# Optimization experiments

Hardware: AMD Instinct MI355X
Metric: run time of the kernel (lower is better)

The kernel has to match this reference:

```python
import jax, jax.numpy as jnp
import numpy as np

ALPHA = 0.2  # LeakyReLU negative slope
NEG = -9e15

def _gat_head(Wh, a1, a2, adj_mask):
    # Wh: [N,O], a1/a2: [O], adj_mask: [N,N] bool
    e = jax.nn.leaky_relu(jnp.einsum('no,o->n', Wh, a1)[:, None]
                          + jnp.einsum('no,o->n', Wh, a2)[None, :], ALPHA)
    att = jax.nn.softmax(jnp.where(adj_mask, e, NEG), axis=-1)
    return att @ Wh  # [N,O]

def setup_inputs() -> dict:
    key = jax.random.key(0)
    ks = jax.random.split(key, 6)
    N, F_IN, O, H, C = 4096, 512, 64, 8, 16
    x = jax.random.normal(ks[0], (N, F_IN), jnp.float32)
    adj = jax.random.randint(ks[1], (N, N), 0, 2, jnp.int32)
    W = jax.random.normal(ks[2], (H, F_IN, O), jnp.float32) * 0.05
    a = jax.random.normal(ks[3], (H, 2 * O), jnp.float32) * 0.05
    W_out = jax.random.normal(ks[4], (H * O, C), jnp.float32) * 0.05
    a_out = jax.random.normal(ks[5], (2 * C,), jnp.float32) * 0.05
    return {'x': x, 'adj': adj, 'W': W, 'a': a, 'W_out': W_out, 'a_out': a_out}

def reference(x, adj, W, a, W_out, a_out):
    N = x.shape[0]
    H, _, O = W.shape
    C = W_out.shape[1]
    mask = adj > 0  # [N,N]
    # multi-head attention layer (vmapped over heads)
    Wh = jnp.einsum('nf,hfo->hno', x, W)  # [H,N,O]
    a1, a2 = a[:, :O], a[:, O:]
    h_heads = jax.vmap(_gat_head, in_axes=(0, 0, 0, None))(Wh, a1, a2, mask)  # [H,N,O]
    h = jax.nn.elu(h_heads)  # concat=True -> elu per head
    h = jnp.transpose(h, (1, 0, 2)).reshape(N, H * O)  # concat heads
    # output attention layer (concat=False)
    Wh_o = h @ W_out  # [N,C]
    out = _gat_head(Wh_o, a_out[:C], a_out[C:], mask)  # [N,C]
    out = jax.nn.elu(out)
    return jax.nn.log_softmax(out, axis=1)
```

## Files before the change

### kernel.cpp

```cpp
#include <hip/hip_runtime.h>


typedef __attribute__((ext_vector_type(8))) short short8;
typedef __attribute__((ext_vector_type(4))) float f32x4;
typedef unsigned long long u64;
typedef unsigned short u16;
typedef unsigned int u32;

__device__ __forceinline__ u16 f2bf_rne(float f){
  u32 u = __float_as_uint(f);
  return (u16)((u + 0x7fffu + ((u >> 16) & 1u)) >> 16);
}
__device__ __forceinline__ void async16(void* lds, const void* g){
  __builtin_amdgcn_global_load_lds((const __attribute__((address_space(1))) u32*)g,
                                   (__attribute__((address_space(3))) u32*)lds, 16, 0, 0);
}

__global__ __launch_bounds__(256) void k_prep(const float* __restrict__ x,
                                              const float* __restrict__ W,
                                              u16* __restrict__ xA,
                                              u16* __restrict__ wB){
  if (blockIdx.x < 1024){
    int t = blockIdx.x * 256 + threadIdx.x;
    int n = t & 4095, fg = t >> 12;
    const float* src = x + (size_t)n * 512 + fg * 8;
    float4 v0 = ((const float4*)src)[0];
    float4 v1 = ((const float4*)src)[1];
    u32 pk[4];
    pk[0] = f2bf_rne(v0.x) | ((u32)f2bf_rne(v0.y) << 16);
    pk[1] = f2bf_rne(v0.z) | ((u32)f2bf_rne(v0.w) << 16);
    pk[2] = f2bf_rne(v1.x) | ((u32)f2bf_rne(v1.y) << 16);
    pk[3] = f2bf_rne(v1.z) | ((u32)f2bf_rne(v1.w) << 16);
    *(uint4*)(xA + ((size_t)fg * 4096 + n) * 8) = *(uint4*)pk;
  } else {
    int t = (blockIdx.x - 1024) * 256 + threadIdx.x;
    int o = t & 63, fg = (t >> 6) & 63, h = t >> 12;
    const float* src = W + ((size_t)h * 512 + fg * 8) * 64 + o;
    u32 pk[4];
    #pragma unroll
    for (int p = 0; p < 4; ++p){
      u16 lo = f2bf_rne(src[(2 * p) * 64]);
      u16 hi = f2bf_rne(src[(2 * p + 1) * 64]);
      pk[p] = lo | ((u32)hi << 16);
    }
    *(uint4*)(wB + (size_t)h * 32768 + ((size_t)fg * 64 + o) * 8) = *(uint4*)pk;
  }
}

__global__ __launch_bounds__(256) void k_gemm1(const u16* __restrict__ xA,
                                               const u16* __restrict__ wB,
                                               const float* __restrict__ av,
                                               const int* __restrict__ adj,
                                               u16* __restrict__ whB,
                                               u64* __restrict__ bits_t,
                                               float* __restrict__ r1,
                                               float* __restrict__ e21, float* __restrict__ e202){
  __shared__ u16 tr[4096];
  int h    = blockIdx.y;
  int nblk = blockIdx.x;
  int lane = threadIdx.x & 63;
  int wv   = threadIdx.x >> 6;
  int row16 = lane & 15, grp = lane >> 4;
  int n0 = nblk * 64;
  int n0w = n0 + wv * 16;
  const u16* wBh = wB + (size_t)h * 32768;
  f32x4 acc[4] = {};
  #pragma unroll 4
  for (int ks = 0; ks < 16; ++ks){
    int fgb = ks * 4 + grp;
    short8 af = *(const short8*)(xA + ((size_t)fgb * 4096 + n0w + row16) * 8);
    #pragma unroll
    for (int nt = 0; nt < 4; ++nt){
      short8 bf = *(const short8*)(wBh + ((size_t)fgb * 64 + nt * 16 + row16) * 8);
      acc[nt] = __builtin_amdgcn_mfma_f32_16x16x32_bf16(af, bf, acc[nt], 0, 0, 0);
    }
  }
  float a1v[4], a2v[4];
  #pragma unroll
  for (int nt = 0; nt < 4; ++nt){
    a1v[nt] = av[h * 128 + nt * 16 + row16];
    a2v[nt] = av[h * 128 + 64 + nt * 16 + row16];
  }
  #pragma unroll
  for (int r = 0; r < 4; ++r){
    float p1 = acc[0][r]*a1v[0] + acc[1][r]*a1v[1] + acc[2][r]*a1v[2] + acc[3][r]*a1v[3];
    float p2 = acc[0][r]*a2v[0] + acc[1][r]*a2v[1] + acc[2][r]*a2v[2] + acc[3][r]*a2v[3];
    #pragma unroll
    for (int d = 1; d < 16; d <<= 1){ p1 += __shfl_xor(p1, d, 64); p2 += __shfl_xor(p2, d, 64); }
    if (row16 == 0){
      int idx = h * 4096 + n0w + grp * 4 + r;
      r1[idx]   = __expf(-0.8f * p1);
      e21[idx]  = __expf(p2);
      e202[idx] = __expf(0.2f * p2);
    }
  }
  #pragma unroll
  for (int nt = 0; nt < 4; ++nt)
    #pragma unroll
    for (int r = 0; r < 4; ++r){
      int jl = wv * 16 + grp * 4 + r;
      int o  = nt * 16 + row16;
      tr[((jl >> 3) * 64 + o) * 8 + (jl & 7)] = f2bf_rne(acc[nt][r]);
    }
  __syncthreads();
  u16* dst = whB + (size_t)h * 262144 + (size_t)n0 * 64;
  #pragma unroll
  for (int q = 0; q < 2; ++q)
    *(uint4*)(dst + (threadIdx.x * 2 + q) * 8) = *(const uint4*)(tr + (threadIdx.x * 2 + q) * 8);

  {
    int B = blockIdx.y * 64 + blockIdx.x;
    int uid0 = B * 512 + wv * 128;
    for (int k = 0; k < 128; k += 8){
      int v[8];
      #pragma unroll
      for (int q = 0; q < 8; ++q){
        int uid = uid0 + k + q;
        v[q] = adj[(size_t)(uid >> 6) * 4096 + ((uid & 63) << 6) + lane];
      }
      u64 m[8];
      #pragma unroll
      for (int q = 0; q < 8; ++q) m[q] = __ballot(v[q] != 0);
      if (lane == 0){
        #pragma unroll
        for (int q = 0; q < 8; ++q){
          int uid = uid0 + k + q;
          bits_t[(size_t)(uid & 63) * 4096 + (uid >> 6)] = m[q];
        }
      }
    }
  }
}

__global__ __launch_bounds__(256) void k_att1(const u16* __restrict__ whB,
                                              const u64* __restrict__ bits_t,
                                              const float* __restrict__ r1,
                                              const float* __restrict__ e21, const float* __restrict__ e202,
                                              u16* __restrict__ pnum, float* __restrict__ pden){
  __shared__ u16  smB[2][4096];
  __shared__ u32  smLut[4];
  int h     = blockIdx.y;
  int iblk  = blockIdx.x;
  int split = blockIdx.z;
  int lane = threadIdx.x & 63;
  int wv   = threadIdx.x >> 6;
  int row16 = lane & 15, grp = lane >> 4;
  if (threadIdx.x < 4)
    smLut[threadIdx.x] = ((threadIdx.x & 1) ? 0xFFFFu : 0u) | ((threadIdx.x & 2) ? 0xFFFF0000u : 0u);
  int i = iblk * 64 + wv * 16 + row16;
  int hoff = h * 4096;
  float r = r1[hoff + i];
  const u16* whBh = whB + (size_t)h * 262144;
  int jbeg = split * 1024;

  short8 bden;
  #pragma unroll
  for (int t = 0; t < 8; ++t) bden[t] = (row16 == 0) ? (short)0x3F80 : (short)0;

  auto stage = [&](int bb, int j0){
    const char* g = (const char*)whBh + (size_t)j0 * 128 + wv * 2048 + lane * 16;
    char* l = (char*)(&smB[bb][0]) + wv * 2048;
    async16(l, g);
    async16(l + 1024, g + 1024);
  };

  f32x4 acc[4] = {};
  f32x4 accden = {};
  stage(0, jbeg);
  for (int c = 0; c < 16; ++c){
    int bb = c & 1;
    int j0 = jbeg + c * 64;
    u64 mrow = bits_t[(size_t)(split * 16 + c) * 4096 + i];
    __syncthreads();
    if (c < 15) stage(bb ^ 1, j0 + 64);
    #pragma unroll
    for (int ks = 0; ks < 2; ++ks){
      const float* t1 = e21  + hoff + j0 + ks * 32 + grp * 8;
      const float* t2 = e202 + hoff + j0 + ks * 32 + grp * 8;
      float4 eA = *(const float4*)t1;
      float4 eB = *(const float4*)(t1 + 4);
      float4 gA = *(const float4*)t2;
      float4 gB = *(const float4*)(t2 + 4);
      float e1v[8] = {eA.x, eA.y, eA.z, eA.w, eB.x, eB.y, eB.z, eB.w};
      float e2v[8] = {gA.x, gA.y, gA.z, gA.w, gB.x, gB.y, gB.z, gB.w};
      const u16* bbase = &smB[bb][(ks * 4 + grp) * 512];
      short8 bf0 = *(const short8*)(bbase + (0 * 16 + row16) * 8);
      short8 bf1 = *(const short8*)(bbase + (1 * 16 + row16) * 8);
      short8 bf2 = *(const short8*)(bbase + (2 * 16 + row16) * 8);
      short8 bf3 = *(const short8*)(bbase + (3 * 16 + row16) * 8);
      u32 mb = ((u32)(mrow >> (ks * 32)) >> (grp * 8)) & 0xffu;
      u32 pk[4];
      #pragma unroll
      for (int t2i = 0; t2i < 4; ++t2i){
        float w0 = fmaxf(e1v[2 * t2i],     r * e2v[2 * t2i]);
        float w1 = fmaxf(e1v[2 * t2i + 1], r * e2v[2 * t2i + 1]);
        u32 p = __builtin_amdgcn_perm(__float_as_uint(w1), __float_as_uint(w0), 0x07060302u);
        pk[t2i] = p & smLut[(mb >> (2 * t2i)) & 3u];
      }
      short8 af = *(short8*)pk;
      acc[0] = __builtin_amdgcn_mfma_f32_16x16x32_bf16(af, bf0, acc[0], 0, 0, 0);
      acc[1] = __builtin_amdgcn_mfma_f32_16x16x32_bf16(af, bf1, acc[1], 0, 0, 0);
      acc[2] = __builtin_amdgcn_mfma_f32_16x16x32_bf16(af, bf2, acc[2], 0, 0, 0);
      acc[3] = __builtin_amdgcn_mfma_f32_16x16x32_bf16(af, bf3, acc[3], 0, 0, 0);
      accden = __builtin_amdgcn_mfma_f32_16x16x32_bf16(af, bden, accden, 0, 0, 0);
    }
  }

  #pragma unroll
  for (int r4 = 0; r4 < 4; ++r4){
    int n = iblk * 64 + wv * 16 + grp * 4 + r4;
    if (row16 == 0)
      pden[((size_t)split * 8 + h) * 4096 + n] = accden[r4];
    u16* dst = pnum + ((size_t)split * 4096 + n) * 512 + h * 64 + row16;
    #pragma unroll
    for (int nt = 0; nt < 4; ++nt)
      dst[nt * 16] = f2bf_rne(acc[nt][r4]);
  }
}

__global__ __launch_bounds__(256) void k_gemm2(const u16* __restrict__ pnum,
                                               const float* __restrict__ pden,
                                               const float* __restrict__ Wout,
                                               const float* __restrict__ aout,
                                               u16* __restrict__ whoB,
                                               float* __restrict__ r1o,
                                               float* __restrict__ e21o, float* __restrict__ e202o){
  __shared__ float Wl[8192];
  __shared__ float hrow[16 * 516];
  __shared__ float sden[128];
  int n0 = blockIdx.x * 16;
  for (int t = threadIdx.x; t < 8192; t += 256) Wl[t] = Wout[t];
  if (threadIdx.x < 128){
    int hh = threadIdx.x >> 4, nn = threadIdx.x & 15;
    float d = 0.f;
    #pragma unroll
    for (int s = 0; s < 4; ++s) d += pden[((size_t)s * 8 + hh) * 4096 + n0 + nn];
    sden[threadIdx.x] = d;
  }
  __syncthreads();
  {
    int nn = threadIdx.x >> 4;
    int fc = threadIdx.x & 15;
    int f0 = fc * 32;
    int hh = fc >> 1;
    float dinv = 1.f / sden[hh * 16 + nn];
    float v[32];
    #pragma unroll
    for (int k = 0; k < 32; ++k) v[k] = 0.f;
    #pragma unroll
    for (int s = 0; s < 4; ++s){
      const u16* p = pnum + ((size_t)s * 4096 + n0 + nn) * 512 + f0;
      #pragma unroll
      for (int q = 0; q < 4; ++q){
        uint4 raw = *(const uint4*)(p + q * 8);
        u32 rw[4] = {raw.x, raw.y, raw.z, raw.w};
        #pragma unroll
        for (int d2 = 0; d2 < 4; ++d2){
          v[q * 8 + d2 * 2]     += __uint_as_float(rw[d2] << 16);
          v[q * 8 + d2 * 2 + 1] += __uint_as_float(rw[d2] & 0xffff0000u);
        }
      }
    }
    #pragma unroll
    for (int k = 0; k < 32; ++k){
      float val = v[k] * dinv;
      val = val > 0.f ? val : (__expf(val) - 1.f);
      hrow[nn * 516 + f0 + k] = val;
    }
  }
  __syncthreads();
  int c  = threadIdx.x & 15;
  int rl = threadIdx.x >> 4;
  int n = n0 + rl;
  const float4* hr = (const float4*)(hrow + rl * 516);
  float acc = 0.f;
  #pragma unroll 8
  for (int f4 = 0; f4 < 128; ++f4){
    float4 hv = hr[f4];
    int f = f4 * 4;
    acc += hv.x * Wl[f * 16 + c] + hv.y * Wl[(f + 1) * 16 + c]
         + hv.z * Wl[(f + 2) * 16 + c] + hv.w * Wl[(f + 3) * 16 + c];
  }
  whoB[((size_t)(n >> 3) * 16 + c) * 8 + (n & 7)] = f2bf_rne(acc);
  float p1 = acc * aout[c], p2 = acc * aout[16 + c];
  #pragma unroll
  for (int d = 1; d < 16; d <<= 1){ p1 += __shfl_xor(p1, d, 64); p2 += __shfl_xor(p2, d, 64); }
  if (c == 0){
    r1o[n]   = __expf(-0.8f * p1);
    e21o[n]  = __expf(p2);
    e202o[n] = __expf(0.2f * p2);
  }
}

__global__ __launch_bounds__(256) void k_att2f(const u16* __restrict__ whoB,
                                               const u64* __restrict__ bits_t,
                                               const float* __restrict__ r1o,
                                               const float* __restrict__ e21o, const float* __restrict__ e202o,
                                               float* __restrict__ out){
  __shared__ float s_acc[4][16][16];
  __shared__ float s_den[4][16];
  __shared__ u32 smLut[4];
  int n0 = blockIdx.x * 16;
  int tid = threadIdx.x;
  int lane = tid & 63, wv = tid >> 6;
  int row16 = lane & 15, grp = lane >> 4;
  if (tid < 4)
    smLut[tid] = ((tid & 1) ? 0xFFFFu : 0u) | ((tid & 2) ? 0xFFFF0000u : 0u);
  __syncthreads();
  int i = n0 + row16;
  float r = r1o[i];
  short8 bden;
  #pragma unroll
  for (int t = 0; t < 8; ++t) bden[t] = (row16 == 0) ? (short)0x3F80 : (short)0;

  f32x4 acc = {};
  f32x4 accden = {};
  int jbase = wv * 1024;
  for (int c = 0; c < 16; ++c){
    int j0 = jbase + c * 64;
    u64 mrow = bits_t[(size_t)(wv * 16 + c) * 4096 + i];
    #pragma unroll
    for (int ks = 0; ks < 2; ++ks){
      int sb = (j0 >> 3) + ks * 4 + grp;
      short8 bf = *(const short8*)(whoB + ((size_t)sb * 16 + row16) * 8);
      const float* t1 = e21o  + j0 + ks * 32 + grp * 8;
      const float* t2 = e202o + j0 + ks * 32 + grp * 8;
      float4 eA = *(const float4*)t1;
      float4 eB = *(const float4*)(t1 + 4);
      float4 gA = *(const float4*)t2;
      float4 gB = *(const float4*)(t2 + 4);
      float e1v[8] = {eA.x, eA.y, eA.z, eA.w, eB.x, eB.y, eB.z, eB.w};
      float e2v[8] = {gA.x, gA.y, gA.z, gA.w, gB.x, gB.y, gB.z, gB.w};
      u32 mb = ((u32)(mrow >> (ks * 32)) >> (grp * 8)) & 0xffu;
      u32 pk[4];
      #pragma unroll
      for (int t2i = 0; t2i < 4; ++t2i){
        float w0 = fmaxf(e1v[2 * t2i],     r * e2v[2 * t2i]);
        float w1 = fmaxf(e1v[2 * t2i + 1], r * e2v[2 * t2i + 1]);
        u32 p = __builtin_amdgcn_perm(__float_as_uint(w1), __float_as_uint(w0), 0x07060302u);
        pk[t2i] = p & smLut[(mb >> (2 * t2i)) & 3u];
      }
      short8 af = *(short8*)pk;
      acc    = __builtin_amdgcn_mfma_f32_16x16x32_bf16(af, bf, acc, 0, 0, 0);
      accden = __builtin_amdgcn_mfma_f32_16x16x32_bf16(af, bden, accden, 0, 0, 0);
    }
  }
  #pragma unroll
  for (int r4 = 0; r4 < 4; ++r4){
    s_acc[wv][grp * 4 + r4][row16] = acc[r4];
    if (row16 == 0) s_den[wv][grp * 4 + r4] = accden[r4];
  }
  __syncthreads();
  {
    int row = tid >> 4, c = tid & 15;
    float num = s_acc[0][row][c] + s_acc[1][row][c] + s_acc[2][row][c] + s_acc[3][row][c];
    float den = s_den[0][row] + s_den[1][row] + s_den[2][row] + s_den[3][row];
    float v = num / den;
    v = v > 0.f ? v : (__expf(v) - 1.f);
    float m = v;
    #pragma unroll
    for (int d = 1; d < 16; d <<= 1) m = fmaxf(m, __shfl_xor(m, d, 64));
    float es = __expf(v - m), ss = es;
    #pragma unroll
    for (int d = 1; d < 16; d <<= 1) ss += __shfl_xor(ss, d, 64);
    out[(size_t)(n0 + row) * 16 + c] = v - m - __logf(ss);
  }
}

extern "C" void kernel_launch(void* const* d_in, const int* in_sizes, int n_in,
                              void* d_out, int out_size, void* d_ws, size_t ws_size,
                              hipStream_t stream){
  (void)in_sizes; (void)n_in; (void)out_size; (void)ws_size;
  const float* x    = (const float*)d_in[0];
  const int*   adj  = (const int*)d_in[1];
  const float* W    = (const float*)d_in[2];
  const float* av   = (const float*)d_in[3];
  const float* Wout = (const float*)d_in[4];
  const float* aout = (const float*)d_in[5];
  float* out = (float*)d_out;
  char* ws = (char*)d_ws;

  u64*  bits_t  = (u64*)(ws + 0x0000000);
  u16*  whB     = (u16*)(ws + 0x0200000);
  float* r1     = (float*)(ws + 0x0600000);
  float* e21    = (float*)(ws + 0x0620000);
  float* e202   = (float*)(ws + 0x0640000);
  u16*  xA      = (u16*)(ws + 0x0680000);
  u16*  wB      = (u16*)(ws + 0x0A80000);
  u16*  pnum1   = (u16*)(ws + 0x0680000);
  float* pden1  = (float*)(ws + 0x1680000);
  u16*  whoB    = (u16*)(ws + 0x1700000);
  float* r1o    = (float*)(ws + 0x1720000);
  float* e21o   = (float*)(ws + 0x1724000);
  float* e202o  = (float*)(ws + 0x1728000);

  k_prep<<<dim3(1152), dim3(256), 0, stream>>>(x, W, xA, wB);
  k_gemm1<<<dim3(64, 8), dim3(256), 0, stream>>>(xA, wB, av, adj, whB, bits_t, r1, e21, e202);
  k_att1<<<dim3(64, 8, 4), dim3(256), 0, stream>>>(whB, bits_t, r1, e21, e202, pnum1, pden1);
  k_gemm2<<<dim3(256), dim3(256), 0, stream>>>(pnum1, pden1, Wout, aout, whoB, r1o, e21o, e202o);
  k_att2f<<<dim3(256), dim3(256), 0, stream>>>(whoB, bits_t, r1o, e21o, e202o, out);
}
```

Measured before the change: 207.2 us.

## Fuse input conversion into gemm1, switch to fp16 packed math, split att2

Removes the prep kernel by converting W into LDS and x on the fly inside gemm1. Switches all MFMA operands from bf16 to fp16, stores the exp tables as fp16, and computes attention weights with packed half2 max/mul. att1 now stages the exp tables into LDS asynchronously. att2 is split across 16 column chunks with a separate final reduction kernel for more parallelism. The risks are redundant per-block W conversion, repeated fp32 reads of x for each head, and fp16 range limits on the exponentials.

```diff
diff --git a/kernel.cpp b/kernel.cpp
--- a/kernel.cpp
+++ b/kernel.cpp
@@ -1,78 +1,80 @@
 #include <hip/hip_runtime.h>
-
-
-typedef __attribute__((ext_vector_type(8))) short short8;
+#include <string.h>
+
+
+typedef _Float16 h2 __attribute__((ext_vector_type(2)));
+typedef _Float16 half8 __attribute__((ext_vector_type(8)));
 typedef __attribute__((ext_vector_type(4))) float f32x4;
 typedef unsigned long long u64;
 typedef unsigned short u16;
 typedef unsigned int u32;
 
-__device__ __forceinline__ u16 f2bf_rne(float f){
-  u32 u = __float_as_uint(f);
-  return (u16)((u + 0x7fffu + ((u >> 16) & 1u)) >> 16);
-}
+__device__ __forceinline__ u16 f2h(float f){
+  union { _Float16 h; u16 u; } c; c.h = (_Float16)f; return c.u;
+}
+__device__ __forceinline__ h2 u2h2(u32 u){ union { u32 u; h2 h; } c; c.u = u; return c.h; }
+__device__ __forceinline__ u32 h22u(h2 h){ union { u32 u; h2 h; } c; c.h = h; return c.u; }
+__device__ __forceinline__ half8 pk2h8(uint4 v){ union { uint4 u; half8 h; } c; c.u = v; return c.h; }
+
 __device__ __forceinline__ void async16(void* lds, const void* g){
   __builtin_amdgcn_global_load_lds((const __attribute__((address_space(1))) u32*)g,
                                    (__attribute__((address_space(3))) u32*)lds, 16, 0, 0);
 }
-
-__global__ __launch_bounds__(256) void k_prep(const float* __restrict__ x,
-                                              const float* __restrict__ W,
-                                              u16* __restrict__ xA,
-                                              u16* __restrict__ wB){
-  if (blockIdx.x < 1024){
-    int t = blockIdx.x * 256 + threadIdx.x;
-    int n = t & 4095, fg = t >> 12;
-    const float* src = x + (size_t)n * 512 + fg * 8;
-    float4 v0 = ((const float4*)src)[0];
-    float4 v1 = ((const float4*)src)[1];
-    u32 pk[4];
-    pk[0] = f2bf_rne(v0.x) | ((u32)f2bf_rne(v0.y) << 16);
-    pk[1] = f2bf_rne(v0.z) | ((u32)f2bf_rne(v0.w) << 16);
-    pk[2] = f2bf_rne(v1.x) | ((u32)f2bf_rne(v1.y) << 16);
-    pk[3] = f2bf_rne(v1.z) | ((u32)f2bf_rne(v1.w) << 16);
-    *(uint4*)(xA + ((size_t)fg * 4096 + n) * 8) = *(uint4*)pk;
-  } else {
-    int t = (blockIdx.x - 1024) * 256 + threadIdx.x;
-    int o = t & 63, fg = (t >> 6) & 63, h = t >> 12;
-    const float* src = W + ((size_t)h * 512 + fg * 8) * 64 + o;
-    u32 pk[4];
-    #pragma unroll
-    for (int p = 0; p < 4; ++p){
-      u16 lo = f2bf_rne(src[(2 * p) * 64]);
-      u16 hi = f2bf_rne(src[(2 * p + 1) * 64]);
-      pk[p] = lo | ((u32)hi << 16);
-    }
-    *(uint4*)(wB + (size_t)h * 32768 + ((size_t)fg * 64 + o) * 8) = *(uint4*)pk;
-  }
-}
-
-__global__ __launch_bounds__(256) void k_gemm1(const u16* __restrict__ xA,
-                                               const u16* __restrict__ wB,
+__device__ __forceinline__ void async4(void* lds, const void* g){
+  __builtin_amdgcn_global_load_lds((const __attribute__((address_space(1))) u32*)g,
+                                   (__attribute__((address_space(3))) u32*)lds, 4, 0, 0);
+}
+
+__global__ __launch_bounds__(256) void k_gemm1(const float* __restrict__ x,
+                                               const float* __restrict__ W,
                                                const float* __restrict__ av,
                                                const int* __restrict__ adj,
                                                u16* __restrict__ whB,
                                                u64* __restrict__ bits_t,
                                                float* __restrict__ r1,
-                                               float* __restrict__ e21, float* __restrict__ e202){
+                                               u16* __restrict__ e21h, u16* __restrict__ e202h){
+  __shared__ u16 wLDS[32768];
   __shared__ u16 tr[4096];
   int h    = blockIdx.y;
   int nblk = blockIdx.x;
-  int lane = threadIdx.x & 63;
-  int wv   = threadIdx.x >> 6;
+  int tid  = threadIdx.x;
+  int lane = tid & 63;
+  int wv   = tid >> 6;
   int row16 = lane & 15, grp = lane >> 4;
   int n0 = nblk * 64;
   int n0w = n0 + wv * 16;
-  const u16* wBh = wB + (size_t)h * 32768;
+
+  {
+    int o = tid & 63, fb0 = tid >> 6;
+    for (int k = 0; k < 16; ++k){
+      int fgb = fb0 + k * 4;
+      const float* src = W + ((size_t)h * 512 + fgb * 8) * 64 + o;
+      u32 pk[4];
+      #pragma unroll
+      for (int p = 0; p < 4; ++p)
+        pk[p] = (u32)f2h(src[(2 * p) * 64]) | ((u32)f2h(src[(2 * p + 1) * 64]) << 16);
+      *(uint4*)(wLDS + ((size_t)fgb * 64 + o) * 8) = *(uint4*)pk;
+    }
+  }
+  __syncthreads();
+
   f32x4 acc[4] = {};
   #pragma unroll 4
   for (int ks = 0; ks < 16; ++ks){
     int fgb = ks * 4 + grp;
-    short8 af = *(const short8*)(xA + ((size_t)fgb * 4096 + n0w + row16) * 8);
+    const float* xs = x + (size_t)(n0w + row16) * 512 + fgb * 8;
+    float4 xv0 = ((const float4*)xs)[0];
+    float4 xv1 = ((const float4*)xs)[1];
+    u32 ax[4];
+    ax[0] = (u32)f2h(xv0.x) | ((u32)f2h(xv0.y) << 16);
+    ax[1] = (u32)f2h(xv0.z) | ((u32)f2h(xv0.w) << 16);
+    ax[2] = (u32)f2h(xv1.x) | ((u32)f2h(xv1.y) << 16);
+    ax[3] = (u32)f2h(xv1.z) | ((u32)f2h(xv1.w) << 16);
+    half8 af = pk2h8(*(uint4*)ax);
     #pragma unroll
     for (int nt = 0; nt < 4; ++nt){
-      short8 bf = *(const short8*)(wBh + ((size_t)fgb * 64 + nt * 16 + row16) * 8);
-      acc[nt] = __builtin_amdgcn_mfma_f32_16x16x32_bf16(af, bf, acc[nt], 0, 0, 0);
+      half8 bf = *(const half8*)(wLDS + ((size_t)fgb * 64 + nt * 16 + row16) * 8);
+      acc[nt] = __builtin_amdgcn_mfma_f32_16x16x32_f16(af, bf, acc[nt], 0, 0, 0);
     }
   }
   float a1v[4], a2v[4];
@@ -89,9 +91,9 @@
     for (int d = 1; d < 16; d <<= 1){ p1 += __shfl_xor(p1, d, 64); p2 += __shfl_xor(p2, d, 64); }
     if (row16 == 0){
       int idx = h * 4096 + n0w + grp * 4 + r;
-      r1[idx]   = __expf(-0.8f * p1);
-      e21[idx]  = __expf(p2);
-      e202[idx] = __expf(0.2f * p2);
+      r1[idx]    = __expf(-0.8f * p1);
+      e21h[idx]  = f2h(__expf(p2));
+      e202h[idx] = f2h(__expf(0.2f * p2));
     }
   }
   #pragma unroll
@@ -100,13 +102,13 @@
     for (int r = 0; r < 4; ++r){
       int jl = wv * 16 + grp * 4 + r;
       int o  = nt * 16 + row16;
-      tr[((jl >> 3) * 64 + o) * 8 + (jl & 7)] = f2bf_rne(acc[nt][r]);
+      tr[((jl >> 3) * 64 + o) * 8 + (jl & 7)] = f2h(acc[nt][r]);
     }
   __syncthreads();
   u16* dst = whB + (size_t)h * 262144 + (size_t)n0 * 64;
   #pragma unroll
   for (int q = 0; q < 2; ++q)
-    *(uint4*)(dst + (threadIdx.x * 2 + q) * 8) = *(const uint4*)(tr + (threadIdx.x * 2 + q) * 8);
+    *(uint4*)(dst + (tid * 2 + q) * 8) = *(const uint4*)(tr + (tid * 2 + q) * 8);
 
   {
     int B = blockIdx.y * 64 + blockIdx.x;
@@ -135,9 +137,10 @@
 __global__ __launch_bounds__(256) void k_att1(const u16* __restrict__ whB,
                                               const u64* __restrict__ bits_t,
                                               const float* __restrict__ r1,
-                                              const float* __restrict__ e21, const float* __restrict__ e202,
+                                              const u16* __restrict__ e21h, const u16* __restrict__ e202h,
                                               u16* __restrict__ pnum, float* __restrict__ pden){
   __shared__ u16  smB[2][4096];
+  __shared__ u32  smT[2][2][64];
   __shared__ u32  smLut[4];
   int h     = blockIdx.y;
   int iblk  = blockIdx.x;
@@ -149,19 +152,25 @@
     smLut[threadIdx.x] = ((threadIdx.x & 1) ? 0xFFFFu : 0u) | ((threadIdx.x & 2) ? 0xFFFF0000u : 0u);
   int i = iblk * 64 + wv * 16 + row16;
   int hoff = h * 4096;
-  float r = r1[hoff + i];
+  u32 rb = (u32)f2h(r1[hoff + i]); rb |= rb << 16;
+  h2 rr = u2h2(rb);
   const u16* whBh = whB + (size_t)h * 262144;
   int jbeg = split * 1024;
 
-  short8 bden;
-  #pragma unroll
-  for (int t = 0; t < 8; ++t) bden[t] = (row16 == 0) ? (short)0x3F80 : (short)0;
+  half8 bden;
+  {
+    u32 z[4] = {0,0,0,0};
+    if (row16 == 0){ z[0]=0x3C003C00u; z[1]=0x3C003C00u; z[2]=0x3C003C00u; z[3]=0x3C003C00u; }
+    bden = pk2h8(*(uint4*)z);
+  }
 
   auto stage = [&](int bb, int j0){
     const char* g = (const char*)whBh + (size_t)j0 * 128 + wv * 2048 + lane * 16;
     char* l = (char*)(&smB[bb][0]) + wv * 2048;
     async16(l, g);
     async16(l + 1024, g + 1024);
+    if (wv == 0)      async4(&smT[bb][0][0], (const char*)(e21h  + hoff + j0) + lane * 4);
+    else if (wv == 1) async4(&smT[bb][1][0], (const char*)(e202h + hoff + j0) + lane * 4);
   };
 
   f32x4 acc[4] = {};
@@ -169,40 +178,33 @@
   stage(0, jbeg);
   for (int c = 0; c < 16; ++c){
     int bb = c & 1;
-    int j0 = jbeg + c * 64;
     u64 mrow = bits_t[(size_t)(split * 16 + c) * 4096 + i];
     __syncthreads();
-    if (c < 15) stage(bb ^ 1, j0 + 64);
+    if (c < 15) stage(bb ^ 1, jbeg + (c + 1) * 64);
     #pragma unroll
     for (int ks = 0; ks < 2; ++ks){
-      const float* t1 = e21  + hoff + j0 + ks * 32 + grp * 8;
-      const float* t2 = e202 + hoff + j0 + ks * 32 + grp * 8;
-      float4 eA = *(const float4*)t1;
-      float4 eB = *(const float4*)(t1 + 4);
-      float4 gA = *(const float4*)t2;
-      float4 gB = *(const float4*)(t2 + 4);
-      float e1v[8] = {eA.x, eA.y, eA.z, eA.w, eB.x, eB.y, eB.z, eB.w};
-      float e2v[8] = {gA.x, gA.y, gA.z, gA.w, gB.x, gB.y, gB.z, gB.w};
+      uint4 e1q = *(const uint4*)((const char*)&smT[bb][0][0] + ks * 64 + grp * 16);
+      uint4 e2q = *(const uint4*)((const char*)&smT[bb][1][0] + ks * 64 + grp * 16);
+      u32 es[4] = {e1q.x, e1q.y, e1q.z, e1q.w};
+      u32 gs[4] = {e2q.x, e2q.y, e2q.z, e2q.w};
       const u16* bbase = &smB[bb][(ks * 4 + grp) * 512];
-      short8 bf0 = *(const short8*)(bbase + (0 * 16 + row16) * 8);
-      short8 bf1 = *(const short8*)(bbase + (1 * 16 + row16) * 8);
-      short8 bf2 = *(const short8*)(bbase + (2 * 16 + row16) * 8);
-      short8 bf3 = *(const short8*)(bbase + (3 * 16 + row16) * 8);
+      half8 bf0 = *(const half8*)(bbase + (0 * 16 + row16) * 8);
+      half8 bf1 = *(const half8*)(bbase + (1 * 16 + row16) * 8);
+      half8 bf2 = *(const half8*)(bbase + (2 * 16 + row16) * 8);
+      half8 bf3 = *(const half8*)(bbase + (3 * 16 + row16) * 8);
       u32 mb = ((u32)(mrow >> (ks * 32)) >> (grp * 8)) & 0xffu;
       u32 pk[4];
       #pragma unroll
       for (int t2i = 0; t2i < 4; ++t2i){
-        float w0 = fmaxf(e1v[2 * t2i],     r * e2v[2 * t2i]);
-        float w1 = fmaxf(e1v[2 * t2i + 1], r * e2v[2 * t2i + 1]);
-        u32 p = __builtin_amdgcn_perm(__float_as_uint(w1), __float_as_uint(w0), 0x07060302u);
-        pk[t2i] = p & smLut[(mb >> (2 * t2i)) & 3u];
+        h2 w = __builtin_elementwise_max(u2h2(es[t2i]), rr * u2h2(gs[t2i]));
+        pk[t2i] = h22u(w) & smLut[(mb >> (2 * t2i)) & 3u];
       }
-      short8 af = *(short8*)pk;
-      acc[0] = __builtin_amdgcn_mfma_f32_16x16x32_bf16(af, bf0, acc[0], 0, 0, 0);
-      acc[1] = __builtin_amdgcn_mfma_f32_16x16x32_bf16(af, bf1, acc[1], 0, 0, 0);
-      acc[2] = __builtin_amdgcn_mfma_f32_16x16x32_bf16(af, bf2, acc[2], 0, 0, 0);
-      acc[3] = __builtin_amdgcn_mfma_f32_16x16x32_bf16(af, bf3, acc[3], 0, 0, 0);
-      accden = __builtin_amdgcn_mfma_f32_16x16x32_bf16(af, bden, accden, 0, 0, 0);
+      half8 af = pk2h8(*(uint4*)pk);
+      acc[0] = __builtin_amdgcn_mfma_f32_16x16x32_f16(af, bf0, acc[0], 0, 0, 0);
+      acc[1] = __builtin_amdgcn_mfma_f32_16x16x32_f16(af, bf1, acc[1], 0, 0, 0);
+      acc[2] = __builtin_amdgcn_mfma_f32_16x16x32_f16(af, bf2, acc[2], 0, 0, 0);
+      acc[3] = __builtin_amdgcn_mfma_f32_16x16x32_f16(af, bf3, acc[3], 0, 0, 0);
+      accden = __builtin_amdgcn_mfma_f32_16x16x32_f16(af, bden, accden, 0, 0, 0);
     }
   }
 
@@ -214,7 +216,7 @@
     u16* dst = pnum + ((size_t)split * 4096 + n) * 512 + h * 64 + row16;
     #pragma unroll
     for (int nt = 0; nt < 4; ++nt)
-      dst[nt * 16] = f2bf_rne(acc[nt][r4]);
+      dst[nt * 16] = f2h(acc[nt][r4]);
   }
 }
 
@@ -224,7 +226,7 @@
                                                const float* __restrict__ aout,
                                                u16* __restrict__ whoB,
                                                float* __restrict__ r1o,
-                                               float* __restrict__ e21o, float* __restrict__ e202o){
+                                               u16* __restrict__ e21oh, u16* __restrict__ e202oh){
   __shared__ float Wl[8192];
   __shared__ float hrow[16 * 516];
   __shared__ float sden[128];
@@ -256,8 +258,9 @@
         u32 rw[4] = {raw.x, raw.y, raw.z, raw.w};
         #pragma unroll
         for (int d2 = 0; d2 < 4; ++d2){
-          v[q * 8 + d2 * 2]     += __uint_as_float(rw[d2] << 16);
-          v[q * 8 + d2 * 2 + 1] += __uint_as_float(rw[d2] & 0xffff0000u);
+          h2 dh = u2h2(rw[d2]);
+          v[q * 8 + d2 * 2]     += (float)dh.x;
+          v[q * 8 + d2 * 2 + 1] += (float)dh.y;
         }
       }
     }
@@ -281,90 +284,98 @@
     acc += hv.x * Wl[f * 16 + c] + hv.y * Wl[(f + 1) * 16 + c]
          + hv.z * Wl[(f + 2) * 16 + c] + hv.w * Wl[(f + 3) * 16 + c];
   }
-  whoB[((size_t)(n >> 3) * 16 + c) * 8 + (n & 7)] = f2bf_rne(acc);
+  whoB[((size_t)(n >> 3) * 16 + c) * 8 + (n & 7)] = f2h(acc);
   float p1 = acc * aout[c], p2 = acc * aout[16 + c];
   #pragma unroll
   for (int d = 1; d < 16; d <<= 1){ p1 += __shfl_xor(p1, d, 64); p2 += __shfl_xor(p2, d, 64); }
   if (c == 0){
-    r1o[n]   = __expf(-0.8f * p1);
-    e21o[n]  = __expf(p2);
-    e202o[n] = __expf(0.2f * p2);
-  }
-}
-
-__global__ __launch_bounds__(256) void k_att2f(const u16* __restrict__ whoB,
-                                               const u64* __restrict__ bits_t,
-                                               const float* __restrict__ r1o,
-                                               const float* __restrict__ e21o, const float* __restrict__ e202o,
-                                               float* __restrict__ out){
-  __shared__ float s_acc[4][16][16];
-  __shared__ float s_den[4][16];
+    r1o[n]    = __expf(-0.8f * p1);
+    e21oh[n]  = f2h(__expf(p2));
+    e202oh[n] = f2h(__expf(0.2f * p2));
+  }
+}
+
+__global__ __launch_bounds__(256) void k_att2(const u16* __restrict__ whoB,
+                                              const u64* __restrict__ bits_t,
+                                              const float* __restrict__ r1o,
+                                              const u16* __restrict__ e21oh, const u16* __restrict__ e202oh,
+                                              float* __restrict__ pnum, float* __restrict__ pden){
   __shared__ u32 smLut[4];
-  int n0 = blockIdx.x * 16;
-  int tid = threadIdx.x;
-  int lane = tid & 63, wv = tid >> 6;
+  int iblk  = blockIdx.x;
+  int split = blockIdx.y;
+  int lane = threadIdx.x & 63;
+  int wv   = threadIdx.x >> 6;
   int row16 = lane & 15, grp = lane >> 4;
-  if (tid < 4)
-    smLut[tid] = ((tid & 1) ? 0xFFFFu : 0u) | ((tid & 2) ? 0xFFFF0000u : 0u);
+  if (threadIdx.x < 4)
+    smLut[threadIdx.x] = ((threadIdx.x & 1) ? 0xFFFFu : 0u) | ((threadIdx.x & 2) ? 0xFFFF0000u : 0u);
   __syncthreads();
-  int i = n0 + row16;
-  float r = r1o[i];
-  short8 bden;
-  #pragma unroll
-  for (int t = 0; t < 8; ++t) bden[t] = (row16 == 0) ? (short)0x3F80 : (short)0;
+  int i = iblk * 64 + wv * 16 + row16;
+  u32 rb = (u32)f2h(r1o[i]); rb |= rb << 16;
+  h2 rr = u2h2(rb);
+  int jbeg = split * 256;
+  half8 bden;
+  {
+    u32 z[4] = {0,0,0,0};
+    if (row16 == 0){ z[0]=0x3C003C00u; z[1]=0x3C003C00u; z[2]=0x3C003C00u; z[3]=0x3C003C00u; }
+    bden = pk2h8(*(uint4*)z);
+  }
 
   f32x4 acc = {};
   f32x4 accden = {};
-  int jbase = wv * 1024;
-  for (int c = 0; c < 16; ++c){
-    int j0 = jbase + c * 64;
-    u64 mrow = bits_t[(size_t)(wv * 16 + c) * 4096 + i];
+  #pragma unroll
+  for (int c = 0; c < 4; ++c){
+    int j0 = jbeg + c * 64;
+    u64 mrow = bits_t[(size_t)(split * 4 + c) * 4096 + i];
     #pragma unroll
     for (int ks = 0; ks < 2; ++ks){
       int sb = (j0 >> 3) + ks * 4 + grp;
-      short8 bf = *(const short8*)(whoB + ((size_t)sb * 16 + row16) * 8);
-      const float* t1 = e21o  + j0 + ks * 32 + grp * 8;
-      const float* t2 = e202o + j0 + ks * 32 + grp * 8;
-      float4 eA = *(const float4*)t1;
-      float4 eB = *(const float4*)(t1 + 4);
-      float4 gA = *(const float4*)t2;
-      float4 gB = *(const float4*)(t2 + 4);
-      float e1v[8] = {eA.x, eA.y, eA.z, eA.w, eB.x, eB.y, eB.z, eB.w};
-      float e2v[8] = {gA.x, gA.y, gA.z, gA.w, gB.x, gB.y, gB.z, gB.w};
+      half8 bf = *(const half8*)(whoB + ((size_t)sb * 16 + row16) * 8);
+      uint4 e1q = *(const uint4*)(e21oh  + j0 + ks * 32 + grp * 8);
+      uint4 e2q = *(const uint4*)(e202oh + j0 + ks * 32 + grp * 8);
+      u32 es[4] = {e1q.x, e1q.y, e1q.z, e1q.w};
+      u32 gs[4] = {e2q.x, e2q.y, e2q.z, e2q.w};
       u32 mb = ((u32)(mrow >> (ks * 32)) >> (grp * 8)) & 0xffu;
       u32 pk[4];
       #pragma unroll
       for (int t2i = 0; t2i < 4; ++t2i){
-        float w0 = fmaxf(e1v[2 * t2i],     r * e2v[2 * t2i]);
-        float w1 = fmaxf(e1v[2 * t2i + 1], r * e2v[2 * t2i + 1]);
-        u32 p = __builtin_amdgcn_perm(__float_as_uint(w1), __float_as_uint(w0), 0x07060302u);
-        pk[t2i] = p & smLut[(mb >> (2 * t2i)) & 3u];
+        h2 w = __builtin_elementwise_max(u2h2(es[t2i]), rr * u2h2(gs[t2i]));
+        pk[t2i] = h22u(w) & smLut[(mb >> (2 * t2i)) & 3u];
       }
-      short8 af = *(short8*)pk;
-      acc    = __builtin_amdgcn_mfma_f32_16x16x32_bf16(af, bf, acc, 0, 0, 0);
-      accden = __builtin_amdgcn_mfma_f32_16x16x32_bf16(af, bden, accden, 0, 0, 0);
+      half8 af = pk2h8(*(uint4*)pk);
+      acc    = __builtin_amdgcn_mfma_f32_16x16x32_f16(af, bf, acc, 0, 0, 0);
+      accden = __builtin_amdgcn_mfma_f32_16x16x32_f16(af, bden, accden, 0, 0, 0);
     }
   }
   #pragma unroll
   for (int r4 = 0; r4 < 4; ++r4){
-    s_acc[wv][grp * 4 + r4][row16] = acc[r4];
-    if (row16 == 0) s_den[wv][grp * 4 + r4] = accden[r4];
-  }
-  __syncthreads();
-  {
-    int row = tid >> 4, c = tid & 15;
-    float num = s_acc[0][row][c] + s_acc[1][row][c] + s_acc[2][row][c] + s_acc[3][row][c];
-    float den = s_den[0][row] + s_den[1][row] + s_den[2][row] + s_den[3][row];
-    float v = num / den;
-    v = v > 0.f ? v : (__expf(v) - 1.f);
-    float m = v;
-    #pragma unroll
-    for (int d = 1; d < 16; d <<= 1) m = fmaxf(m, __shfl_xor(m, d, 64));
-    float es = __expf(v - m), ss = es;
-    #pragma unroll
-    for (int d = 1; d < 16; d <<= 1) ss += __shfl_xor(ss, d, 64);
-    out[(size_t)(n0 + row) * 16 + c] = v - m - __logf(ss);
-  }
+    int n = iblk * 64 + wv * 16 + grp * 4 + r4;
+    if (row16 == 0)
+      pden[(size_t)n * 16 + split] = accden[r4];
+    pnum[((size_t)n * 16 + split) * 16 + row16] = acc[r4];
+  }
+}
+
+__global__ __launch_bounds__(256) void k_final(const float* __restrict__ pnum,
+                                               const float* __restrict__ pden,
+                                               float* __restrict__ out){
+  int tid = blockIdx.x * 256 + threadIdx.x;
+  int c = tid & 15;
+  int n = tid >> 4;
+  float num = 0.f, den = 0.f;
+  #pragma unroll
+  for (int s = 0; s < 16; ++s){
+    num += pnum[((size_t)n * 16 + s) * 16 + c];
+    den += pden[(size_t)n * 16 + s];
+  }
+  float v = num / den;
+  v = v > 0.f ? v : (__expf(v) - 1.f);
+  float m = v;
+  #pragma unroll
+  for (int d = 1; d < 16; d <<= 1) m = fmaxf(m, __shfl_xor(m, d, 64));
+  float es = __expf(v - m), ss = es;
+  #pragma unroll
+  for (int d = 1; d < 16; d <<= 1) ss += __shfl_xor(ss, d, 64);
+  out[(size_t)n * 16 + c] = v - m - __logf(ss);
 }
 
 extern "C" void kernel_launch(void* const* d_in, const int* in_sizes, int n_in,
@@ -383,20 +394,20 @@
   u64*  bits_t  = (u64*)(ws + 0x0000000);
   u16*  whB     = (u16*)(ws + 0x0200000);
   float* r1     = (float*)(ws + 0x0600000);
-  float* e21    = (float*)(ws + 0x0620000);
-  float* e202   = (float*)(ws + 0x0640000);
-  u16*  xA      = (u16*)(ws + 0x0680000);
-  u16*  wB      = (u16*)(ws + 0x0A80000);
+  u16*  e21h    = (u16*)(ws + 0x0620000);
+  u16*  e202h   = (u16*)(ws + 0x0630000);
   u16*  pnum1   = (u16*)(ws + 0x0680000);
   float* pden1  = (float*)(ws + 0x1680000);
   u16*  whoB    = (u16*)(ws + 0x1700000);
   float* r1o    = (float*)(ws + 0x1720000);
-  float* e21o   = (float*)(ws + 0x1724000);
-  float* e202o  = (float*)(ws + 0x1728000);
-
-  k_prep<<<dim3(1152), dim3(256), 0, stream>>>(x, W, xA, wB);
-  k_gemm1<<<dim3(64, 8), dim3(256), 0, stream>>>(xA, wB, av, adj, whB, bits_t, r1, e21, e202);
-  k_att1<<<dim3(64, 8, 4), dim3(256), 0, stream>>>(whB, bits_t, r1, e21, e202, pnum1, pden1);
-  k_gemm2<<<dim3(256), dim3(256), 0, stream>>>(pnum1, pden1, Wout, aout, whoB, r1o, e21o, e202o);
-  k_att2f<<<dim3(256), dim3(256), 0, stream>>>(whoB, bits_t, r1o, e21o, e202o, out);
-}
+  u16*  e21oh   = (u16*)(ws + 0x1724000);
+  u16*  e202oh  = (u16*)(ws + 0x1726000);
+  float* pnum2  = (float*)(ws + 0x1730000);
+  float* pden2  = (float*)(ws + 0x1B30000);
+
+  k_gemm1<<<dim3(64, 8), dim3(256), 0, stream>>>(x, W, av, adj, whB, bits_t, r1, e21h, e202h);
+  k_att1<<<dim3(64, 8, 4), dim3(256), 0, stream>>>(whB, bits_t, r1, e21h, e202h, pnum1, pden1);
+  k_gemm2<<<dim3(256), dim3(256), 0, stream>>>(pnum1, pden1, Wout, aout, whoB, r1o, e21oh, e202oh);
+  k_att2<<<dim3(64, 16), dim3(256), 0, stream>>>(whoB, bits_t, r1o, e21oh, e202oh, pnum2, pden2);
+  k_final<<<dim3(256), dim3(256), 0, stream>>>(pnum2, pden2, out);
+}
```

Result: faster. 175.4 us (-15.4%).
